# Optimization experiments

Measured on AMD Instinct MI355X. Metric: run time of the kernel, lower is better.

## Reference

```python
import jax, jax.numpy as jnp
import numpy as np

B, C, CI, H, W = 4, 128, 64, 96, 96  # batch, in_channels, inter_channels, spatial
SS = 2                                # sub_sample_factor (maxpool on phi and g)
BN_EPS = 1e-5


def conv1x1(x, w, b):
    # x: [B,C,H,W], w: [O,C], b: [O]
    return jnp.einsum('bchw,oc->bohw', x, w) + b[None, :, None, None]


def maxpool2(x):
    # 2x2 max pool, stride 2. x: [B,C,H,W]
    b, c, h, w = x.shape
    return x.reshape(b, c, h // 2, 2, w // 2, 2).max(axis=(3, 5))


def setup_inputs() -> dict:
    key = jax.random.key(0)
    ks = jax.random.split(key, 12)
    s_in = 1.0 / np.sqrt(C)
    s_ci = 1.0 / np.sqrt(CI)
    return {
        'x':        jax.random.normal(ks[0], (B, C, H, W), jnp.float32),
        'g_w':      jax.random.normal(ks[1], (CI, C), jnp.float32) * s_in,
        'g_b':      jax.random.normal(ks[2], (CI,), jnp.float32) * 0.01,
        'theta_w':  jax.random.normal(ks[3], (CI, C), jnp.float32) * s_in,
        'theta_b':  jax.random.normal(ks[4], (CI,), jnp.float32) * 0.01,
        'phi_w':    jax.random.normal(ks[5], (CI, C), jnp.float32) * s_in,
        'phi_b':    jax.random.normal(ks[6], (CI,), jnp.float32) * 0.01,
        'W_w':      jax.random.normal(ks[7], (C, CI), jnp.float32) * s_ci,
        'W_b':      jax.random.normal(ks[8], (C,), jnp.float32) * 0.01,
        'bn_gamma': jax.random.normal(ks[9], (C,), jnp.float32) * 0.1 + 1.0,
        'bn_beta':  jax.random.normal(ks[10], (C,), jnp.float32) * 0.1,
        'bn_mean':  jax.random.normal(ks[11], (C,), jnp.float32) * 0.1,
        'bn_var':   jax.random.uniform(jax.random.fold_in(key, 99), (C,), jnp.float32, 0.5, 1.5),
    }


def reference(x, g_w, g_b, theta_w, theta_b, phi_w, phi_b, W_w, W_b,
              bn_gamma, bn_beta, bn_mean, bn_var):
    b = x.shape[0]
    # g: conv1x1 -> maxpool(2) -> [B, N_kv, CI]
    g_x = maxpool2(conv1x1(x, g_w, g_b)).reshape(b, CI, -1).transpose(0, 2, 1)
    # theta: conv1x1 -> [B, N_q, CI]
    theta_x = conv1x1(x, theta_w, theta_b).reshape(b, CI, -1).transpose(0, 2, 1)
    # phi: conv1x1 -> maxpool(2) -> [B, CI, N_kv]
    phi_x = maxpool2(conv1x1(x, phi_w, phi_b)).reshape(b, CI, -1)
    # full affinity [B, N_q, N_kv], softmax over keys (embedded_gaussian)
    f = jnp.einsum('bqc,bck->bqk', theta_x, phi_x)
    attn = jax.nn.softmax(f, axis=-1)
    y = jnp.einsum('bqk,bkc->bqc', attn, g_x)            # [B, N_q, CI]
    y = y.transpose(0, 2, 1).reshape(b, CI, H, W)
    # W: conv1x1 (CI -> C) + BatchNorm (inference form) + residual
    W_y = conv1x1(y, W_w, W_b)
    inv = bn_gamma * jax.lax.rsqrt(bn_var + BN_EPS)
    W_y = W_y * inv[None, :, None, None] + (bn_beta - bn_mean * inv)[None, :, None, None]
    return W_y + x
```

## Files before the change

kernel.cpp:

```cpp
#include <hip/hip_runtime.h>
#include <hip/hip_bf16.h>

#define NB 4
#define NC 128
#define NH 96
#define NQ 9216
#define NKV 2304

typedef __bf16 bf8 __attribute__((ext_vector_type(8)));
typedef float f4 __attribute__((ext_vector_type(4)));
typedef unsigned short u16t;
typedef unsigned int u32t;
typedef u32t u32x2 __attribute__((ext_vector_type(2)));

static __device__ __forceinline__ u16t f2bf(float f){
  u32t u = __builtin_bit_cast(u32t, f);
  u = (u + 0x7fffu + ((u >> 16) & 1u)) >> 16;
  return (u16t)u;
}

static __device__ __forceinline__ f4 mfma16(bf8 a, bf8 b, f4 c){
  return __builtin_amdgcn_mfma_f32_16x16x32_bf16(a, b, c, 0, 0, 0);
}

#define GLDS16(gp, lp) __builtin_amdgcn_global_load_lds( \
    (const u32t*)(gp), (u32t*)(lp), 16, 0, 0)

__global__ __launch_bounds__(256) void prep_weights(
    const float* __restrict__ g_w, const float* __restrict__ theta_w,
    const float* __restrict__ phi_w, const float* __restrict__ W_w,
    const float* __restrict__ W_b, const float* __restrict__ bn_gamma,
    const float* __restrict__ bn_beta, const float* __restrict__ bn_mean,
    const float* __restrict__ bn_var,
    u16t* __restrict__ wt_theta, u16t* __restrict__ wt_phi,
    u16t* __restrict__ wt_g, u16t* __restrict__ wt_W,
    float* __restrict__ alpha, float* __restrict__ beta2)
{
  int i = blockIdx.x * 256 + threadIdx.x;
  wt_theta[i] = f2bf(theta_w[i]);
  wt_phi[i]   = f2bf(phi_w[i]);
  wt_g[i]     = f2bf(g_w[i]);
  wt_W[i]     = f2bf(W_w[i]);
  if (blockIdx.x == 0 && threadIdx.x < 128){
    int t = threadIdx.x;
    float inv = bn_gamma[t] * rsqrtf(bn_var[t] + 1e-5f);
    alpha[t] = inv;
    beta2[t] = W_b[t]*inv + bn_beta[t] - bn_mean[t]*inv;
  }
}

__global__ __launch_bounds__(256) void conv3_pool(
    const float* __restrict__ x,
    const u16t* __restrict__ wt_theta, const u16t* __restrict__ wt_phi,
    const u16t* __restrict__ wt_g,
    const float* __restrict__ theta_b, const float* __restrict__ phi_b,
    const float* __restrict__ g_b,
    u16t* __restrict__ theta, u16t* __restrict__ phi, u16t* __restrict__ g_t)
{
  __shared__ __align__(16) u16t xt[64][136];
  const int blk = blockIdx.x;
  const int batch = blk / 144;
  const int t144 = blk % 144;
  const int ph = t144 / 3;
  const int pw0 = (t144 % 3) * 16;
  const int t = threadIdx.x;
  const float* xb = x + (size_t)batch * NC * NQ;

  #pragma unroll
  for (int i = 0; i < 8; ++i){
    int slot = i*256 + t;
    int c = slot >> 4;
    int quad = slot & 15;
    int row = quad >> 3, col4 = (quad & 7)*4;
    int q = (ph*2 + row)*NH + pw0*2 + col4;
    float4 v = *(const float4*)&xb[(size_t)c*NQ + q];
    int pl = row*32 + col4;
    xt[pl+0][c] = f2bf(v.x);
    xt[pl+1][c] = f2bf(v.y);
    xt[pl+2][c] = f2bf(v.z);
    xt[pl+3][c] = f2bf(v.w);
  }
  __syncthreads();

  const int w = t >> 6, l = t & 63, lm = l & 15, lg = l >> 4;
  auto PL = [](int pxi){
    return (((pxi>>1)&1) << 5) + 8*(pxi>>4) + 2*((pxi>>2)&3) + (pxi&1);
  };
  auto QROW = [&](int pxi){
    return (ph*2 + ((pxi>>1)&1))*NH + (pw0 + 4*(pxi>>4) + ((pxi>>2)&3))*2 + (pxi&1);
  };
  bf8 a[4];
  #pragma unroll
  for (int k = 0; k < 4; ++k)
    a[k] = *(const bf8*)&xt[PL(w*16 + lm)][k*32 + lg*8];

  const int kv = ph*48 + pw0 + 4*w + lg;

  f4 Dth[4];
  #pragma unroll
  for (int s = 0; s < 4; ++s){
    float bv = theta_b[s*16 + lm];
    f4 D = {bv, bv, bv, bv};
    #pragma unroll
    for (int k = 0; k < 4; ++k){
      bf8 b = *(const bf8*)&wt_theta[(s*16 + lm)*128 + k*32 + lg*8];
      D = mfma16(a[k], b, D);
    }
    Dth[s] = D;
  }
  {
    u16t* pp = phi + (size_t)batch * NKV * 64;
    #pragma unroll
    for (int s = 0; s < 4; ++s){
      float bv = phi_b[s*16 + lm];
      f4 D = {bv, bv, bv, bv};
      #pragma unroll
      for (int k = 0; k < 4; ++k){
        bf8 b = *(const bf8*)&wt_phi[(s*16 + lm)*128 + k*32 + lg*8];
        D = mfma16(a[k], b, D);
      }
      float mx = fmaxf(fmaxf(D[0], D[1]), fmaxf(D[2], D[3]));
      pp[(size_t)kv*64 + s*16 + lm] = f2bf(mx);
    }
  }
  {
    u16t* gt = g_t + (size_t)batch * 64 * NKV;
    #pragma unroll
    for (int s = 0; s < 4; ++s){
      float bv = g_b[s*16 + lm];
      f4 D = {bv, bv, bv, bv};
      #pragma unroll
      for (int k = 0; k < 4; ++k){
        bf8 b = *(const bf8*)&wt_g[(s*16 + lm)*128 + k*32 + lg*8];
        D = mfma16(a[k], b, D);
      }
      float mx = fmaxf(fmaxf(D[0], D[1]), fmaxf(D[2], D[3]));
      gt[(size_t)(s*16 + lm)*NKV + kv] = f2bf(mx);
    }
  }

  __syncthreads();
  u16t* tl = &xt[0][0];
  #pragma unroll
  for (int s = 0; s < 4; ++s)
    #pragma unroll
    for (int r = 0; r < 4; ++r)
      tl[(w*16 + lg*4 + r)*72 + s*16 + lm] = f2bf(Dth[s][r]);
  __syncthreads();
  {
    u16t* th = theta + (size_t)batch * NQ * 64;
    #pragma unroll
    for (int p = 0; p < 2; ++p){
      int slot = t + 256*p;
      int row = slot >> 3, piece = slot & 7;
      int q = QROW(row);
      *(bf8*)&th[(size_t)q*64 + piece*8] = *(const bf8*)&tl[row*72 + piece*8];
    }
  }
}

#define PHI_OFF 0
#define G_OFF   49152
#define P_OFF   98304
#define SCRAP_OFF 139776

__global__ __launch_bounds__(384) void attn_fused(
    const u16t* __restrict__ theta, const u16t* __restrict__ phi,
    const u16t* __restrict__ g_t, const u16t* __restrict__ wt_W,
    const float* __restrict__ alpha, const float* __restrict__ beta2,
    const float* __restrict__ x, float* __restrict__ out)
{
  __shared__ __align__(16) char SM[143872];
  __shared__ float sums[2][144];

  const int bid = blockIdx.x;
  const int blk = (bid & 7)*32 + (bid >> 3);
  const int batch = blk >> 6;
  const int qb = (blk & 63) * 144;
  const int t = threadIdx.x;
  const int w = t >> 6, l = t & 63, lm = l & 15, lg = l >> 4;
  const int qw = w >> 1, kh = w & 1;

  const u16t* th = theta + ((size_t)batch*NQ + qb)*64;
  bf8 a[3][2];
  #pragma unroll
  for (int mr = 0; mr < 3; ++mr){
    a[mr][0] = *(const bf8*)&th[(qw*48 + mr*16 + lm)*64 + lg*8];
    a[mr][1] = *(const bf8*)&th[(qw*48 + mr*16 + lm)*64 + 32 + lg*8];
  }
  asm volatile("s_waitcnt vmcnt(0)" ::: "memory");

  const char* phc = (const char*)(phi + (size_t)batch*NKV*64);
  const char* gtc = (const char*)(g_t + (size_t)batch*64*NKV);

  auto STAGE = [&](int kt_s, int bufc){
    #pragma unroll
    for (int j = 0; j < 6; ++j){
      int u = w*6 + j;
      int ur = (u < 32) ? u : (u - 32);
      int khu = ur >> 4, isg = (ur >> 3) & 1, sub = ur & 7;
      int row = sub*8 + (l >> 3);
      int swz = ((l & 7) ^ (l >> 3)) << 4;
      int kb = (khu*18 + kt_s) * 64;
      char* dst = (u < 32)
        ? SM + (isg ? G_OFF : PHI_OFF) + (khu*3 + bufc)*8192 + sub*1024 + l*16
        : SM + SCRAP_OFF + (u - 32)*1024 + l*16;
      const char* src = isg
        ? gtc + (size_t)row*(NKV*2) + (size_t)kb*2 + swz
        : phc + (size_t)(kb + row)*128 + swz;
      GLDS16(src, dst);
    }
  };

  f4 Y[3][4];
  #pragma unroll
  for (int mr = 0; mr < 3; ++mr)
    #pragma unroll
    for (int s = 0; s < 4; ++s)
      Y[mr][s] = f4{0.f, 0.f, 0.f, 0.f};
  float lsum[3] = {0.f, 0.f, 0.f};

  u16t* Prow = (u16t*)(SM + P_OFF + w*6912);

  STAGE(0, 0);
  STAGE(1, 1);

  int bufc = 0;
  for (int kt = 0; kt < 18; ++kt){
    __builtin_amdgcn_s_barrier();
    if (kt < 16){
      STAGE(kt + 2, (bufc == 0) ? 2 : bufc - 1);
      asm volatile("s_waitcnt vmcnt(12)" ::: "memory");
    } else if (kt == 16){
      asm volatile("s_waitcnt vmcnt(6)" ::: "memory");
    } else {
      asm volatile("s_waitcnt vmcnt(0)" ::: "memory");
    }
    __builtin_amdgcn_s_barrier();

    const char* pb = SM + PHI_OFF + (kh*3 + bufc)*8192;
    const char* gb = SM + G_OFF   + (kh*3 + bufc)*8192;

    bf8 bp[4][2];
    #pragma unroll
    for (int tt = 0; tt < 4; ++tt){
      int rb = (tt*16 + lm)*128;
      int m7 = lm & 7;
      bp[tt][0] = *(const bf8*)(pb + rb + ((lg ^ m7) << 4));
      bp[tt][1] = *(const bf8*)(pb + rb + (((4 + lg) ^ m7) << 4));
    }
    bf8 bg[4][2];
    #pragma unroll
    for (int s = 0; s < 4; ++s){
      int rb = (s*16 + lm)*128;
      int m7 = lm & 7;
      bg[s][0] = *(const bf8*)(gb + rb + ((lg ^ m7) << 4));
      bg[s][1] = *(const bf8*)(gb + rb + (((4 + lg) ^ m7) << 4));
    }
    f4 S[3][4];
    __builtin_amdgcn_s_setprio(1);
    #pragma unroll
    for (int tt = 0; tt < 4; ++tt)
      #pragma unroll
      for (int mr = 0; mr < 3; ++mr){
        f4 z = {0.f, 0.f, 0.f, 0.f};
        z = mfma16(bp[tt][0], a[mr][0], z);
        S[mr][tt] = mfma16(bp[tt][1], a[mr][1], z);
      }
    __builtin_amdgcn_s_setprio(0);
    #pragma unroll
    for (int mr = 0; mr < 3; ++mr)
      #pragma unroll
      for (int tt = 0; tt < 4; ++tt){
        float p0, p1, p2, p3;
        float a0 = fmaf(S[mr][tt][0], 1.44269504f, -43.2808512f);
        float a1 = fmaf(S[mr][tt][1], 1.44269504f, -43.2808512f);
        float a2 = fmaf(S[mr][tt][2], 1.44269504f, -43.2808512f);
        float a3 = fmaf(S[mr][tt][3], 1.44269504f, -43.2808512f);
        asm("v_exp_f32 %0, %1" : "=v"(p0) : "v"(a0));
        asm("v_exp_f32 %0, %1" : "=v"(p1) : "v"(a1));
        asm("v_exp_f32 %0, %1" : "=v"(p2) : "v"(a2));
        asm("v_exp_f32 %0, %1" : "=v"(p3) : "v"(a3));
        lsum[mr] += (p0 + p1) + (p2 + p3);
        u32t lo, hi;
        asm("v_cvt_pk_bf16_f32 %0, %1, %2" : "=v"(lo) : "v"(p0), "v"(p1));
        asm("v_cvt_pk_bf16_f32 %0, %1, %2" : "=v"(hi) : "v"(p2), "v"(p3));
        *(u32x2*)&Prow[(mr*16 + lm)*72 + tt*16 + lg*4] = u32x2{lo, hi};
      }
    __builtin_amdgcn_s_setprio(1);
    #pragma unroll
    for (int mr = 0; mr < 3; ++mr){
      bf8 pa0 = *(const bf8*)&Prow[(mr*16 + lm)*72 + lg*8];
      bf8 pa1 = *(const bf8*)&Prow[(mr*16 + lm)*72 + 32 + lg*8];
      #pragma unroll
      for (int s = 0; s < 4; ++s){
        Y[mr][s] = mfma16(pa0, bg[s][0], Y[mr][s]);
        Y[mr][s] = mfma16(pa1, bg[s][1], Y[mr][s]);
      }
    }
    __builtin_amdgcn_s_setprio(0);
    bufc = (bufc == 2) ? 0 : bufc + 1;
  }

  #pragma unroll
  for (int mr = 0; mr < 3; ++mr){
    float sv = lsum[mr];
    sv += __shfl_xor(sv, 16);
    sv += __shfl_xor(sv, 32);
    if (lg == 0) sums[kh][qw*48 + mr*16 + lm] = sv;
  }

  __syncthreads();
  float (*yp)[68] = (float (*)[68])SM;
  if (kh == 0){
    #pragma unroll
    for (int mr = 0; mr < 3; ++mr)
      #pragma unroll
      for (int s = 0; s < 4; ++s)
        #pragma unroll
        for (int r = 0; r < 4; ++r)
          yp[qw*48 + mr*16 + lg*4 + r][s*16 + lm] = Y[mr][s][r];
  }
  __syncthreads();
  if (kh == 1){
    #pragma unroll
    for (int mr = 0; mr < 3; ++mr)
      #pragma unroll
      for (int s = 0; s < 4; ++s)
        #pragma unroll
        for (int r = 0; r < 4; ++r)
          yp[qw*48 + mr*16 + lg*4 + r][s*16 + lm] += Y[mr][s][r];
  }
  __syncthreads();

  u16t* yl = (u16t*)(SM + P_OFF);
  #pragma unroll
  for (int i = 0; i < 12; ++i){
    int p = t + 384*i;
    int q = p >> 5, cp = p & 31;
    float tot = sums[0][q] + sums[1][q];
    float inv = 1.0f / tot;
    float v0 = yp[q][cp*2] * inv;
    float v1 = yp[q][cp*2 + 1] * inv;
    u32t pk;
    asm("v_cvt_pk_bf16_f32 %0, %1, %2" : "=v"(pk) : "v"(v0), "v"(v1));
    *(u32t*)&yl[q*72 + cp*2] = pk;
  }
  __syncthreads();

  float (*ol)[130] = (float (*)[130])SM;
  #pragma unroll
  for (int i = 0; i < 12; ++i){
    int tau = w + 6*i;
    int qt = tau >> 3, ct = tau & 7;
    bf8 ya0 = *(const bf8*)&yl[(qt*16 + lm)*72 + lg*8];
    bf8 ya1 = *(const bf8*)&yl[(qt*16 + lm)*72 + 32 + lg*8];
    const u16t* wr = wt_W + (ct*16 + lm)*64;
    bf8 b0 = *(const bf8*)&wr[lg*8];
    bf8 b1 = *(const bf8*)&wr[lg*8 + 32];
    f4 z = {0.f, 0.f, 0.f, 0.f};
    z = mfma16(ya0, b0, z);
    z = mfma16(ya1, b1, z);
    #pragma unroll
    for (int r = 0; r < 4; ++r)
      ol[qt*16 + lg*4 + r][ct*16 + lm] = z[r];
  }
  __syncthreads();

  const float* xb = x + (size_t)batch*NC*NQ + qb;
  float* ob = out + (size_t)batch*NC*NQ + qb;
  #pragma unroll
  for (int i = 0; i < 12; ++i){
    int idx = t + 384*i;
    int c = idx / 36, qv = idx % 36;
    float4 xv = *(const float4*)&xb[(size_t)c*NQ + qv*4];
    float al = alpha[c], be = beta2[c];
    float4 ov;
    ov.x = ol[qv*4 + 0][c]*al + be + xv.x;
    ov.y = ol[qv*4 + 1][c]*al + be + xv.y;
    ov.z = ol[qv*4 + 2][c]*al + be + xv.z;
    ov.w = ol[qv*4 + 3][c]*al + be + xv.w;
    *(float4*)&ob[(size_t)c*NQ + qv*4] = ov;
  }
}

extern "C" void kernel_launch(void* const* d_in, const int* in_sizes, int n_in,
                              void* d_out, int out_size, void* d_ws, size_t ws_size,
                              hipStream_t stream)
{
  const float* x       = (const float*)d_in[0];
  const float* g_w     = (const float*)d_in[1];
  const float* g_b     = (const float*)d_in[2];
  const float* theta_w = (const float*)d_in[3];
  const float* theta_b = (const float*)d_in[4];
  const float* phi_w   = (const float*)d_in[5];
  const float* phi_b   = (const float*)d_in[6];
  const float* W_w     = (const float*)d_in[7];
  const float* W_b     = (const float*)d_in[8];
  const float* bn_g    = (const float*)d_in[9];
  const float* bn_b    = (const float*)d_in[10];
  const float* bn_m    = (const float*)d_in[11];
  const float* bn_v    = (const float*)d_in[12];
  float* out = (float*)d_out;

  char* ws = (char*)d_ws;
  size_t off = 0;
  u16t* theta = (u16t*)(ws + off); off += (size_t)NB*NQ*64*2;
  u16t* phi   = (u16t*)(ws + off); off += (size_t)NB*NKV*64*2;
  u16t* g_t   = (u16t*)(ws + off); off += (size_t)NB*64*NKV*2;
  u16t* wt_theta = (u16t*)(ws + off); off += 64*128*2;
  u16t* wt_phi   = (u16t*)(ws + off); off += 64*128*2;
  u16t* wt_g     = (u16t*)(ws + off); off += 64*128*2;
  u16t* wt_W     = (u16t*)(ws + off); off += 128*64*2;
  float* alpha = (float*)(ws + off); off += 128*4;
  float* beta2 = (float*)(ws + off); off += 128*4;
  if (off > ws_size) return;

  prep_weights<<<32, 256, 0, stream>>>(g_w, theta_w, phi_w, W_w, W_b,
                                       bn_g, bn_b, bn_m, bn_v,
                                       wt_theta, wt_phi, wt_g, wt_W, alpha, beta2);
  conv3_pool<<<576, 256, 0, stream>>>(x, wt_theta, wt_phi, wt_g,
                                      theta_b, phi_b, g_b, theta, phi, g_t);
  attn_fused<<<256, 384, 0, stream>>>(theta, phi, g_t, wt_W, alpha, beta2, x, out);
}
```

Baseline: 81.02 us.

## Feed softmax probabilities to PV MFMA from registers and permute g layout

```diff
diff --git a/kernel.cpp b/kernel.cpp
--- a/kernel.cpp
+++ b/kernel.cpp
@@ -11,7 +11,8 @@
 typedef float f4 __attribute__((ext_vector_type(4)));
 typedef unsigned short u16t;
 typedef unsigned int u32t;
-typedef u32t u32x2 __attribute__((ext_vector_type(2)));
+typedef u32t u32x4 __attribute__((ext_vector_type(4)));
+typedef u16t u16x4v __attribute__((ext_vector_type(4)));
 
 static __device__ __forceinline__ u16t f2bf(float f){
   u32t u = __builtin_bit_cast(u32t, f);
@@ -94,7 +95,8 @@
   for (int k = 0; k < 4; ++k)
     a[k] = *(const bf8*)&xt[PL(w*16 + lm)][k*32 + lg*8];
 
-  const int kv = ph*48 + pw0 + 4*w + lg;
+  const int kvbase = ph*48 + pw0;
+  const int kv = kvbase + 4*w + lg;
 
   f4 Dth[4];
   #pragma unroll
@@ -123,29 +125,29 @@
       pp[(size_t)kv*64 + s*16 + lm] = f2bf(mx);
     }
   }
-  {
-    u16t* gt = g_t + (size_t)batch * 64 * NKV;
-    #pragma unroll
-    for (int s = 0; s < 4; ++s){
-      float bv = g_b[s*16 + lm];
-      f4 D = {bv, bv, bv, bv};
-      #pragma unroll
-      for (int k = 0; k < 4; ++k){
-        bf8 b = *(const bf8*)&wt_g[(s*16 + lm)*128 + k*32 + lg*8];
-        D = mfma16(a[k], b, D);
-      }
-      float mx = fmaxf(fmaxf(D[0], D[1]), fmaxf(D[2], D[3]));
-      gt[(size_t)(s*16 + lm)*NKV + kv] = f2bf(mx);
-    }
+  float gmx[4];
+  #pragma unroll
+  for (int s = 0; s < 4; ++s){
+    float bv = g_b[s*16 + lm];
+    f4 D = {bv, bv, bv, bv};
+    #pragma unroll
+    for (int k = 0; k < 4; ++k){
+      bf8 b = *(const bf8*)&wt_g[(s*16 + lm)*128 + k*32 + lg*8];
+      D = mfma16(a[k], b, D);
+    }
+    gmx[s] = fmaxf(fmaxf(D[0], D[1]), fmaxf(D[2], D[3]));
   }
 
   __syncthreads();
   u16t* tl = &xt[0][0];
-  #pragma unroll
-  for (int s = 0; s < 4; ++s)
+  u16t* gl = &xt[0][0] + 4608;
+  #pragma unroll
+  for (int s = 0; s < 4; ++s){
     #pragma unroll
     for (int r = 0; r < 4; ++r)
       tl[(w*16 + lg*4 + r)*72 + s*16 + lm] = f2bf(Dth[s][r]);
+    gl[(s*16 + lm)*20 + 4*w + lg] = f2bf(gmx[s]);
+  }
   __syncthreads();
   {
     u16t* th = theta + (size_t)batch * NQ * 64;
@@ -157,12 +159,22 @@
       *(bf8*)&th[(size_t)q*64 + piece*8] = *(const bf8*)&tl[row*72 + piece*8];
     }
   }
+  {
+    u16t* gt = g_t + (size_t)batch * 64 * NKV;
+    int c = t >> 2, L = t & 3;
+    int T = (kvbase >> 4) & 3;
+    int kvg = kvbase & ~63;
+    u16x4v v;
+    #pragma unroll
+    for (int u = 0; u < 4; ++u) v[u] = gl[c*20 + L*4 + u];
+    *(u16x4v*)&gt[(size_t)c*NKV + kvg + (T>>1)*32 + ((T&1)<<2) + L*8] = v;
+  }
 }
 
 #define PHI_OFF 0
 #define G_OFF   49152
-#define P_OFF   98304
-#define SCRAP_OFF 139776
+#define SCRAP_OFF 98304
+#define Y_OFF   76800
 
 __global__ __launch_bounds__(384) void attn_fused(
     const u16t* __restrict__ theta, const u16t* __restrict__ phi,
@@ -170,7 +182,7 @@
     const float* __restrict__ alpha, const float* __restrict__ beta2,
     const float* __restrict__ x, float* __restrict__ out)
 {
-  __shared__ __align__(16) char SM[143872];
+  __shared__ __align__(16) char SM[102400];
   __shared__ float sums[2][144];
 
   const int bid = blockIdx.x;
@@ -220,8 +232,6 @@
       Y[mr][s] = f4{0.f, 0.f, 0.f, 0.f};
   float lsum[3] = {0.f, 0.f, 0.f};
 
-  u16t* Prow = (u16t*)(SM + P_OFF + w*6912);
-
   STAGE(0, 0);
   STAGE(1, 1);
 
@@ -240,12 +250,12 @@
 
     const char* pb = SM + PHI_OFF + (kh*3 + bufc)*8192;
     const char* gb = SM + G_OFF   + (kh*3 + bufc)*8192;
+    const int m7 = lm & 7;
 
     bf8 bp[4][2];
     #pragma unroll
     for (int tt = 0; tt < 4; ++tt){
       int rb = (tt*16 + lm)*128;
-      int m7 = lm & 7;
       bp[tt][0] = *(const bf8*)(pb + rb + ((lg ^ m7) << 4));
       bp[tt][1] = *(const bf8*)(pb + rb + (((4 + lg) ^ m7) << 4));
     }
@@ -253,52 +263,47 @@
     #pragma unroll
     for (int s = 0; s < 4; ++s){
       int rb = (s*16 + lm)*128;
-      int m7 = lm & 7;
       bg[s][0] = *(const bf8*)(gb + rb + ((lg ^ m7) << 4));
       bg[s][1] = *(const bf8*)(gb + rb + (((4 + lg) ^ m7) << 4));
     }
-    f4 S[3][4];
-    __builtin_amdgcn_s_setprio(1);
-    #pragma unroll
-    for (int tt = 0; tt < 4; ++tt)
-      #pragma unroll
-      for (int mr = 0; mr < 3; ++mr){
+
+    #pragma unroll
+    for (int mr = 0; mr < 3; ++mr){
+      f4 S[4];
+      __builtin_amdgcn_s_setprio(1);
+      #pragma unroll
+      for (int tt = 0; tt < 4; ++tt){
         f4 z = {0.f, 0.f, 0.f, 0.f};
         z = mfma16(bp[tt][0], a[mr][0], z);
-        S[mr][tt] = mfma16(bp[tt][1], a[mr][1], z);
+        S[tt] = mfma16(bp[tt][1], a[mr][1], z);
       }
-    __builtin_amdgcn_s_setprio(0);
-    #pragma unroll
-    for (int mr = 0; mr < 3; ++mr)
+      __builtin_amdgcn_s_setprio(0);
+      u32t wq[8];
       #pragma unroll
       for (int tt = 0; tt < 4; ++tt){
         float p0, p1, p2, p3;
-        float a0 = fmaf(S[mr][tt][0], 1.44269504f, -43.2808512f);
-        float a1 = fmaf(S[mr][tt][1], 1.44269504f, -43.2808512f);
-        float a2 = fmaf(S[mr][tt][2], 1.44269504f, -43.2808512f);
-        float a3 = fmaf(S[mr][tt][3], 1.44269504f, -43.2808512f);
+        float a0 = fmaf(S[tt][0], 1.44269504f, -43.2808512f);
+        float a1 = fmaf(S[tt][1], 1.44269504f, -43.2808512f);
+        float a2 = fmaf(S[tt][2], 1.44269504f, -43.2808512f);
+        float a3 = fmaf(S[tt][3], 1.44269504f, -43.2808512f);
         asm("v_exp_f32 %0, %1" : "=v"(p0) : "v"(a0));
         asm("v_exp_f32 %0, %1" : "=v"(p1) : "v"(a1));
         asm("v_exp_f32 %0, %1" : "=v"(p2) : "v"(a2));
         asm("v_exp_f32 %0, %1" : "=v"(p3) : "v"(a3));
         lsum[mr] += (p0 + p1) + (p2 + p3);
-        u32t lo, hi;
-        asm("v_cvt_pk_bf16_f32 %0, %1, %2" : "=v"(lo) : "v"(p0), "v"(p1));
-        asm("v_cvt_pk_bf16_f32 %0, %1, %2" : "=v"(hi) : "v"(p2), "v"(p3));
-        *(u32x2*)&Prow[(mr*16 + lm)*72 + tt*16 + lg*4] = u32x2{lo, hi};
+        asm("v_cvt_pk_bf16_f32 %0, %1, %2" : "=v"(wq[tt*2])   : "v"(p0), "v"(p1));
+        asm("v_cvt_pk_bf16_f32 %0, %1, %2" : "=v"(wq[tt*2+1]) : "v"(p2), "v"(p3));
       }
-    __builtin_amdgcn_s_setprio(1);
-    #pragma unroll
-    for (int mr = 0; mr < 3; ++mr){
-      bf8 pa0 = *(const bf8*)&Prow[(mr*16 + lm)*72 + lg*8];
-      bf8 pa1 = *(const bf8*)&Prow[(mr*16 + lm)*72 + 32 + lg*8];
+      bf8 pa0 = __builtin_bit_cast(bf8, u32x4{wq[0], wq[1], wq[2], wq[3]});
+      bf8 pa1 = __builtin_bit_cast(bf8, u32x4{wq[4], wq[5], wq[6], wq[7]});
+      __builtin_amdgcn_s_setprio(1);
       #pragma unroll
       for (int s = 0; s < 4; ++s){
         Y[mr][s] = mfma16(pa0, bg[s][0], Y[mr][s]);
         Y[mr][s] = mfma16(pa1, bg[s][1], Y[mr][s]);
       }
-    }
-    __builtin_amdgcn_s_setprio(0);
+      __builtin_amdgcn_s_setprio(0);
+    }
     bufc = (bufc == 2) ? 0 : bufc + 1;
   }
 
@@ -333,7 +338,7 @@
   }
   __syncthreads();
 
-  u16t* yl = (u16t*)(SM + P_OFF);
+  u16t* yl = (u16t*)(SM + Y_OFF);
   #pragma unroll
   for (int i = 0; i < 12; ++i){
     int p = t + 384*i;
```

Result: faster. 77.73 us (-4.1%).
